# Kernel tuning notes

Hardware: AMD Instinct MI355X
Metric: run time of the kernel (lower is better)

The kernel has to match this reference:

```python
import jax, jax.numpy as jnp
import numpy as np

E = 512        # embedding_dim
HEADS = 8
PD = 32        # patch_dim
STRIDE = 16    # unfold stride (hard-coded in source)
P = 16         # max regions per image (padded)
NCLS = 3       # num_classes
LN_EPS = 1e-5


def layer_norm(x, g, b):
    mu = x.mean(-1, keepdims=True)
    v = ((x - mu) ** 2).mean(-1, keepdims=True)
    return (x - mu) / jnp.sqrt(v + LN_EPS) * g + b


def patch2vec(x, Wr, br):
    # x: [N, C, PD, PD]; AdaptiveAvgPool3d to (C//4, PD//2, PD//2) with exact
    # integer ratios == block-mean pooling, then Linear(fvector, E).
    N, C, H, W = x.shape
    y = x.reshape(N, C // 4, 4, H // 2, 2, W // 2, 2).mean(axis=(2, 4, 6))
    return y.reshape(N, -1) @ Wr.T + br


def mha(q_in, kv_in, Wqkv, bqkv, Wo, bo):
    # torch nn.MultiheadAttention, batch_first=True
    B, Pq, _ = q_in.shape
    L = kv_in.shape[1]
    hd = E // HEADS
    Wq, Wk, Wv = Wqkv[:E], Wqkv[E:2 * E], Wqkv[2 * E:]
    bq, bk, bv = bqkv[:E], bqkv[E:2 * E], bqkv[2 * E:]
    q = (q_in @ Wq.T + bq).reshape(B, Pq, HEADS, hd)
    k = (kv_in @ Wk.T + bk).reshape(B, L, HEADS, hd)
    v = (kv_in @ Wv.T + bv).reshape(B, L, HEADS, hd)
    scores = jnp.einsum('bphd,blhd->bhpl', q, k) / jnp.sqrt(jnp.asarray(hd, q.dtype))
    attn = jax.nn.softmax(scores, axis=-1)
    out = jnp.einsum('bhpl,blhd->bphd', attn, v).reshape(B, Pq, E)
    return out @ Wo.T + bo


def setup_inputs() -> dict:
    key = jax.random.key(0)
    ks = jax.random.split(key, 12)
    B, C, H, W = 8, 64, 256, 256
    fv = (C // 4) * (PD // 2) * (PD // 2)  # 4096
    s = lambda n: 1.0 / np.sqrt(n)
    return {
        'features': jax.random.normal(ks[0], (B, C, H, W), jnp.float32),
        'probs': jax.random.uniform(ks[1], (B, NCLS, H, W), jnp.float32),
        'patches': jax.random.normal(ks[2], (B, P, C, PD, PD), jnp.float32),
        'masks': jax.random.randint(ks[3], (B, H, W), 0, P + 1, jnp.int32),
        'ln_g': jnp.ones((E,), jnp.float32),
        'ln_b': jnp.zeros((E,), jnp.float32),
        'Wr': jax.random.normal(ks[4], (E, fv), jnp.float32) * s(fv),
        'br': jnp.zeros((E,), jnp.float32),
        'Wqkv': jax.random.normal(ks[5], (3 * E, E), jnp.float32) * s(E),
        'bqkv': jnp.zeros((3 * E,), jnp.float32),
        'Wo': jax.random.normal(ks[6], (E, E), jnp.float32) * s(E),
        'bo': jnp.zeros((E,), jnp.float32),
        'Wm': jax.random.normal(ks[7], (E, E), jnp.float32) * s(E),
        'bm': jnp.zeros((E,), jnp.float32),
        'Wc': jax.random.normal(ks[8], (NCLS - 1, E), jnp.float32) * s(E),
        'bc': jnp.zeros((NCLS - 1,), jnp.float32),
    }


def reference(features, probs, patches, masks, ln_g, ln_b, Wr, br,
              Wqkv, bqkv, Wo, bo, Wm, bm, Wc, bc):
    B, C, H, W = features.shape
    # ---- unfold features into overlapping PDxPD blocks, stride 16 ----
    n = (H - PD) // STRIDE + 1  # 15
    rows = (jnp.arange(n) * STRIDE)[:, None] + jnp.arange(PD)[None, :]  # [n, PD]
    xb = features[:, :, rows, :]          # [B, C, n, PD, W]
    blocks = xb[:, :, :, :, rows]         # [B, C, n, PD, n, PD]
    blocks = blocks.transpose(0, 2, 4, 1, 3, 5).reshape(B, n * n, C, PD, PD)
    L = n * n

    # ---- shared Patch2vec embedding + shared LayerNorm ----
    pe = layer_norm(patch2vec(patches.reshape(B * P, C, PD, PD), Wr, br).reshape(B, P, E), ln_g, ln_b)
    be = layer_norm(patch2vec(blocks.reshape(B * L, C, PD, PD), Wr, br).reshape(B, L, E), ln_g, ln_b)

    # ---- attention + residual MLP ----
    attn = mha(pe, be, Wqkv, bqkv, Wo, bo)
    res = layer_norm(attn + pe, ln_g, ln_b)
    x = jax.nn.gelu(res @ Wm.T + bm, approximate=False) + res
    outs = x @ Wc.T + bc  # [B, P, 2]

    # ---- vectorized masked reclassify (regions are disjoint) ----
    labels = masks  # [B, H, W], 0 = background, 1..P = regions
    seg = (labels.astype(jnp.int32) + jnp.arange(B, dtype=jnp.int32)[:, None, None] * (P + 1)).reshape(-1)
    pr = probs.transpose(0, 2, 3, 1).reshape(-1, NCLS)
    sums = jax.ops.segment_sum(pr, seg, num_segments=B * (P + 1)).reshape(B, P + 1, NCLS)
    cnt = jax.ops.segment_sum(jnp.ones((pr.shape[0],), pr.dtype), seg, num_segments=B * (P + 1)).reshape(B, P + 1)
    mean = sums / jnp.maximum(cnt, 1.0)[..., None] + 1e-6  # orig_mean_logits per region
    ml = mean[:, 1:, :]  # [B, P, NCLS], region labels 1..P <-> logits 0..P-1
    new0 = ml[..., 0] / (0.5 * (ml[..., 1] + ml[..., 2])) * outs.mean(-1)
    newv = jnp.stack([new0, outs[..., 0], outs[..., 1]], axis=-1)  # [B, P, 3]
    newv_full = jnp.concatenate([jnp.zeros((B, 1, NCLS), newv.dtype), newv], axis=1)
    vals = newv_full[jnp.arange(B)[:, None], labels.reshape(B, -1)]  # [B, H*W, 3]
    vals = vals.reshape(B, H, W, NCLS).transpose(0, 3, 1, 2)
    return jnp.where((labels > 0)[:, None, :, :], vals, probs)
```

## Files before the change

kernel.cpp:

```cpp
#include <hip/hip_runtime.h>
#include <stdint.h>


typedef __attribute__((ext_vector_type(8))) short bf16x8;
typedef __attribute__((ext_vector_type(4))) float f32x4;

__device__ __forceinline__ unsigned short f2bf(float x) {
    union { float f; unsigned u; } v; v.f = x;
    unsigned r = v.u + 0x7FFFu + ((v.u >> 16) & 1u);
    return (unsigned short)(r >> 16);
}
__device__ __forceinline__ float bf2f(unsigned short x) {
    union { unsigned u; float f; } v; v.u = ((unsigned)x) << 16; return v.f;
}

__device__ __forceinline__ void g2l16(const unsigned short* g, unsigned short* l) {
    __builtin_amdgcn_global_load_lds(
        (const __attribute__((address_space(1))) unsigned int*)g,
        (__attribute__((address_space(3))) unsigned int*)l, 16, 0, 0);
}

__global__ __launch_bounds__(256) void k_prep(
    const float* __restrict__ f, const float* __restrict__ p,
    const float* __restrict__ Wr, const float* __restrict__ Wqkv,
    const float* __restrict__ Wo, const float* __restrict__ Wm,
    unsigned short* __restrict__ gp, unsigned short* __restrict__ Xb,
    unsigned short* __restrict__ oWr, unsigned short* __restrict__ oWqkv,
    unsigned short* __restrict__ oWo, unsigned short* __restrict__ oWm,
    float* __restrict__ seg)
{
    int blk = blockIdx.x, tid = threadIdx.x;
    if (blk < 8192) {
        if (blk == 0) for (int i = tid; i < 544; i += 256) seg[i] = 0.f;
        unsigned t = blk * 256u + tid;
        unsigned q = t & 127u, r = (t >> 7) & 127u, g = (t >> 14) & 15u, b = t >> 18;
        const float2* f2 = (const float2*)f;
        float s = 0.f;
        unsigned cb = b * 64u + g * 4u;
#pragma unroll
        for (int j = 0; j < 4; ++j)
#pragma unroll
            for (int a = 0; a < 2; ++a) {
                unsigned idx = ((cb + j) * 256u + 2u * r + a) * 256u + 2u * q;
                float2 v = f2[idx >> 1];
                s += v.x + v.y;
            }
        gp[t] = f2bf(s * 0.0625f);
    } else if (blk < 10240) {
        unsigned t = (blk - 8192) * 256u + tid;
        unsigned i = t & 4095u, row = t >> 12;
        unsigned q = i & 15u, r = (i >> 4) & 15u, g = i >> 8;
        const float2* p2 = (const float2*)p;
        float s = 0.f;
        unsigned cb = row * 64u + g * 4u;
#pragma unroll
        for (int j = 0; j < 4; ++j)
#pragma unroll
            for (int a = 0; a < 2; ++a) {
                unsigned idx = ((cb + j) * 32u + 2u * r + a) * 32u + 2u * q;
                float2 v = p2[idx >> 1];
                s += v.x + v.y;
            }
        Xb[(size_t)row * 4096 + i] = f2bf(s * 0.0625f);
    } else {
        int t = (blk - 10240) * 256 + tid;
        const float* src; unsigned short* dst; int i;
        if (t < 524288)      { src = Wr;   dst = oWr;   i = t; }
        else if (t < 720896) { src = Wqkv; dst = oWqkv; i = t - 524288; }
        else if (t < 786432) { src = Wo;   dst = oWo;   i = t - 720896; }
        else                 { src = Wm;   dst = oWm;   i = t - 786432; }
        float4 v = ((const float4*)src)[i];
        ushort4 o;
        o.x = f2bf(v.x); o.y = f2bf(v.y); o.z = f2bf(v.z); o.w = f2bf(v.w);
        ((ushort4*)dst)[i] = o;
    }
}

__global__ __launch_bounds__(256) void k_gather_blocks(
    const unsigned short* __restrict__ Gp, unsigned short* __restrict__ Xb)
{
    unsigned t = blockIdx.x * 256u + threadIdx.x;
    unsigned grp = t & 511u, row_rel = t >> 9;
    unsigned k0 = grp * 8u;
    unsigned g = k0 >> 8, r = (k0 >> 4) & 15u, q0 = k0 & 15u;
    unsigned b = row_rel / 225u;
    unsigned ij = row_rel - b * 225u;
    unsigned i = ij / 15u, j = ij - i * 15u;
    size_t src = ((size_t)(b * 16u + g) * 128u + i * 8u + r) * 128u + j * 8u + q0;
    size_t dst = (size_t)(128u + row_rel) * 4096u + k0;
    *(uint4*)(Xb + dst) = *(const uint4*)(Gp + src);
}

__global__ __launch_bounds__(256) void k_gemm128(
    const unsigned short* __restrict__ A, const unsigned short* __restrict__ Bw,
    const float* __restrict__ bias, float* __restrict__ C,
    int M, int N, int K, int klen)
{
    __shared__ __align__(16) unsigned short As[128 * 32];
    __shared__ __align__(16) unsigned short Bs[128 * 32];
    const int tid = threadIdx.x, w = tid >> 6, lane = tid & 63;
    const int nt = blockIdx.x, mt = blockIdx.y, ks = blockIdx.z;
    const int kbase = ks * klen;
    const int l15 = lane & 15, kq = (lane >> 4) * 8;
    const int wm = (w >> 1) * 64, wn = (w & 1) * 64;
    const int srow0 = w * 32, lrow = lane >> 2, lcol = (lane & 3) * 8;

    f32x4 acc[4][4];
#pragma unroll
    for (int i = 0; i < 4; ++i)
#pragma unroll
        for (int j = 0; j < 4; ++j) acc[i][j] = (f32x4){0.f, 0.f, 0.f, 0.f};

    int arow0 = mt * 128, brow0 = nt * 128;
    for (int k0 = 0; k0 < klen; k0 += 32) {
        int kk = kbase + k0;
#pragma unroll
        for (int c = 0; c < 2; ++c) {
            int r = srow0 + c * 16 + lrow;
            int ga = arow0 + r; if (ga > M - 1) ga = M - 1;
            g2l16(A + (size_t)ga * K + kk + lcol, &As[(srow0 + c * 16) * 32]);
            g2l16(Bw + (size_t)(brow0 + r) * K + kk + lcol, &Bs[(srow0 + c * 16) * 32]);
        }
        __syncthreads();
        bf16x8 af[4], bf[4];
#pragma unroll
        for (int i = 0; i < 4; ++i) {
            af[i] = *(const bf16x8*)&As[(wm + 16 * i + l15) * 32 + kq];
            bf[i] = *(const bf16x8*)&Bs[(wn + 16 * i + l15) * 32 + kq];
        }
#pragma unroll
        for (int i = 0; i < 4; ++i)
#pragma unroll
            for (int j = 0; j < 4; ++j)
                acc[i][j] = __builtin_amdgcn_mfma_f32_16x16x32_bf16(af[i], bf[j], acc[i][j], 0, 0, 0);
        __syncthreads();
    }
    float* Cp = C + (size_t)ks * M * N;
#pragma unroll
    for (int i = 0; i < 4; ++i) {
        int rowb = mt * 128 + wm + i * 16 + (lane >> 4) * 4;
#pragma unroll
        for (int j = 0; j < 4; ++j) {
            int col = nt * 128 + wn + j * 16 + l15;
            float bv = bias ? bias[col] : 0.f;
#pragma unroll
            for (int r = 0; r < 4; ++r) {
                int row = rowb + r;
                if (row < M) Cp[(size_t)row * N + col] = acc[i][j][r] + bv;
            }
        }
    }
}

__global__ __launch_bounds__(256) void k_gemm_nt(
    const unsigned short* __restrict__ A, const unsigned short* __restrict__ Bw,
    const float* __restrict__ bias, float* __restrict__ C,
    int M, int N, int K)
{
    __shared__ __align__(16) unsigned short As[64 * 32];
    __shared__ __align__(16) unsigned short Bs[64 * 32];
    const int tid = threadIdx.x;
    const int bm = blockIdx.y, bn = blockIdx.x;
    const int wave = tid >> 6, lane = tid & 63;
    const int wm = (wave >> 1) * 32, wn = (wave & 1) * 32;
    const int l15 = lane & 15, kq = (lane >> 4) * 8;
    const int srow = tid >> 2, scol = (tid & 3) * 8;
    const unsigned short* Ap = A + (size_t)(bm * 64 + srow) * K + scol;
    const unsigned short* Bp = Bw + (size_t)(bn * 64 + srow) * K + scol;

    f32x4 acc[2][2];
#pragma unroll
    for (int i = 0; i < 2; ++i)
#pragma unroll
        for (int j = 0; j < 2; ++j) acc[i][j] = (f32x4){0.f, 0.f, 0.f, 0.f};

    for (int k0 = 0; k0 < K; k0 += 32) {
        *(uint4*)&As[srow * 32 + scol] = *(const uint4*)(Ap + k0);
        *(uint4*)&Bs[srow * 32 + scol] = *(const uint4*)(Bp + k0);
        __syncthreads();
        bf16x8 a0 = *(const bf16x8*)&As[(wm + l15) * 32 + kq];
        bf16x8 a1 = *(const bf16x8*)&As[(wm + 16 + l15) * 32 + kq];
        bf16x8 b0 = *(const bf16x8*)&Bs[(wn + l15) * 32 + kq];
        bf16x8 b1 = *(const bf16x8*)&Bs[(wn + 16 + l15) * 32 + kq];
        acc[0][0] = __builtin_amdgcn_mfma_f32_16x16x32_bf16(a0, b0, acc[0][0], 0, 0, 0);
        acc[0][1] = __builtin_amdgcn_mfma_f32_16x16x32_bf16(a0, b1, acc[0][1], 0, 0, 0);
        acc[1][0] = __builtin_amdgcn_mfma_f32_16x16x32_bf16(a1, b0, acc[1][0], 0, 0, 0);
        acc[1][1] = __builtin_amdgcn_mfma_f32_16x16x32_bf16(a1, b1, acc[1][1], 0, 0, 0);
        __syncthreads();
    }
#pragma unroll
    for (int it = 0; it < 2; ++it) {
        int rowb = bm * 64 + wm + it * 16 + (lane >> 4) * 4;
#pragma unroll
        for (int iu = 0; iu < 2; ++iu) {
            int col = bn * 64 + wn + iu * 16 + l15;
            float bv = bias[col];
#pragma unroll
            for (int r = 0; r < 4; ++r) {
                int row = rowb + r;
                if (row < M) C[(size_t)row * N + col] = acc[it][iu][r] + bv;
            }
        }
    }
}

__global__ __launch_bounds__(256) void k_lnred(
    const float* __restrict__ Yp, const float* __restrict__ br,
    const float* __restrict__ gg, const float* __restrict__ bb,
    float* __restrict__ outF, unsigned short* __restrict__ outB,
    int rows, int nsplit)
{
    int wave = threadIdx.x >> 6, lane = threadIdx.x & 63;
    int row = blockIdx.x * 4 + wave;
    if (row >= rows) return;
    size_t base = (size_t)row * 512 + lane * 8;
    float v[8];
    { const float* bp = br + lane * 8;
      float4 a = *(const float4*)bp, b = *(const float4*)(bp + 4);
      v[0]=a.x; v[1]=a.y; v[2]=a.z; v[3]=a.w; v[4]=b.x; v[5]=b.y; v[6]=b.z; v[7]=b.w; }
    for (int s = 0; s < nsplit; ++s) {
        const float* xp = Yp + (size_t)s * rows * 512 + base;
        float4 a = *(const float4*)xp, b = *(const float4*)(xp + 4);
        v[0]+=a.x; v[1]+=a.y; v[2]+=a.z; v[3]+=a.w; v[4]+=b.x; v[5]+=b.y; v[6]+=b.z; v[7]+=b.w;
    }
    float s = 0.f;
#pragma unroll
    for (int i = 0; i < 8; ++i) s += v[i];
#pragma unroll
    for (int m = 32; m; m >>= 1) s += __shfl_xor(s, m, 64);
    float mu = s * (1.f / 512.f);
    float sq = 0.f;
#pragma unroll
    for (int i = 0; i < 8; ++i) { float d = v[i] - mu; sq += d * d; }
#pragma unroll
    for (int m = 32; m; m >>= 1) sq += __shfl_xor(sq, m, 64);
    float rstd = rsqrtf(sq * (1.f / 512.f) + 1e-5f);
    const float* gp = gg + lane * 8;
    const float* bp2 = bb + lane * 8;
    float4 g0 = *(const float4*)gp, g1 = *(const float4*)(gp + 4);
    float4 b0 = *(const float4*)bp2, b1 = *(const float4*)(bp2 + 4);
    float ga[8] = {g0.x,g0.y,g0.z,g0.w,g1.x,g1.y,g1.z,g1.w};
    float ba[8] = {b0.x,b0.y,b0.z,b0.w,b1.x,b1.y,b1.z,b1.w};
    float o[8];
#pragma unroll
    for (int i = 0; i < 8; ++i) o[i] = (v[i] - mu) * rstd * ga[i] + ba[i];
    float* ofp = outF + base;
    float4 w0; w0.x=o[0]; w0.y=o[1]; w0.z=o[2]; w0.w=o[3];
    float4 w1; w1.x=o[4]; w1.y=o[5]; w1.z=o[6]; w1.w=o[7];
    *(float4*)ofp = w0; *(float4*)(ofp + 4) = w1;
    unsigned short* obp = outB + base;
    ushort4 u0, u1;
    u0.x=f2bf(o[0]); u0.y=f2bf(o[1]); u0.z=f2bf(o[2]); u0.w=f2bf(o[3]);
    u1.x=f2bf(o[4]); u1.y=f2bf(o[5]); u1.z=f2bf(o[6]); u1.w=f2bf(o[7]);
    ((ushort4*)obp)[0] = u0; ((ushort4*)obp)[1] = u1;
}

__global__ __launch_bounds__(256) void k_ln(
    const float* __restrict__ X, const float* __restrict__ R,
    const float* __restrict__ gg, const float* __restrict__ bb,
    float* __restrict__ outF, unsigned short* __restrict__ outB, int rows)
{
    int wave = threadIdx.x >> 6, lane = threadIdx.x & 63;
    int row = blockIdx.x * 4 + wave;
    if (row >= rows) return;
    size_t base = (size_t)row * 512 + lane * 8;
    const float* xp = X + base;
    float v[8];
    { float4 a = *(const float4*)xp, b = *(const float4*)(xp + 4);
      v[0]=a.x; v[1]=a.y; v[2]=a.z; v[3]=a.w; v[4]=b.x; v[5]=b.y; v[6]=b.z; v[7]=b.w; }
    { const float* rp = R + base;
      float4 a = *(const float4*)rp, b = *(const float4*)(rp + 4);
      v[0]+=a.x; v[1]+=a.y; v[2]+=a.z; v[3]+=a.w; v[4]+=b.x; v[5]+=b.y; v[6]+=b.z; v[7]+=b.w; }
    float s = 0.f;
#pragma unroll
    for (int i = 0; i < 8; ++i) s += v[i];
#pragma unroll
    for (int m = 32; m; m >>= 1) s += __shfl_xor(s, m, 64);
    float mu = s * (1.f / 512.f);
    float sq = 0.f;
#pragma unroll
    for (int i = 0; i < 8; ++i) { float d = v[i] - mu; sq += d * d; }
#pragma unroll
    for (int m = 32; m; m >>= 1) sq += __shfl_xor(sq, m, 64);
    float rstd = rsqrtf(sq * (1.f / 512.f) + 1e-5f);
    const float* gp = gg + lane * 8;
    const float* bp = bb + lane * 8;
    float4 g0 = *(const float4*)gp, g1 = *(const float4*)(gp + 4);
    float4 b0 = *(const float4*)bp, b1 = *(const float4*)(bp + 4);
    float ga[8] = {g0.x,g0.y,g0.z,g0.w,g1.x,g1.y,g1.z,g1.w};
    float ba[8] = {b0.x,b0.y,b0.z,b0.w,b1.x,b1.y,b1.z,b1.w};
    float o[8];
#pragma unroll
    for (int i = 0; i < 8; ++i) o[i] = (v[i] - mu) * rstd * ga[i] + ba[i];
    float* ofp = outF + base;
    float4 w0; w0.x=o[0]; w0.y=o[1]; w0.z=o[2]; w0.w=o[3];
    float4 w1; w1.x=o[4]; w1.y=o[5]; w1.z=o[6]; w1.w=o[7];
    *(float4*)ofp = w0; *(float4*)(ofp + 4) = w1;
    unsigned short* obp = outB + base;
    ushort4 u0, u1;
    u0.x=f2bf(o[0]); u0.y=f2bf(o[1]); u0.z=f2bf(o[2]); u0.w=f2bf(o[3]);
    u1.x=f2bf(o[4]); u1.y=f2bf(o[5]); u1.z=f2bf(o[6]); u1.w=f2bf(o[7]);
    ((ushort4*)obp)[0] = u0; ((ushort4*)obp)[1] = u1;
}

__global__ __launch_bounds__(256) void k_attn(
    const float* __restrict__ QKVp, const float* __restrict__ bqkv,
    unsigned short* __restrict__ attn_bf)
{
    const int b = blockIdx.x, h = blockIdx.y, pz = blockIdx.z;
    const size_t PS = (size_t)1928 * 1536;
    __shared__ __align__(16) float qs[4 * 64];
    __shared__ __align__(16) unsigned short Ks[225 * 68];
    __shared__ __align__(16) unsigned short Vs[225 * 64];
    __shared__ float sc[4 * 225];
    const int t = threadIdx.x;

    {
        int p = t >> 6, d = t & 63;
        size_t idx = (size_t)(b * 16 + pz * 4 + p) * 1536 + h * 64 + d;
        qs[t] = QKVp[idx] + QKVp[PS + idx] + bqkv[h * 64 + d];
    }
    float bk = bqkv[512 + h * 64 + (t & 63)];
    float bv = bqkv[1024 + h * 64 + (t & 63)];
    for (int i = t; i < 14400; i += 256) {
        int l = i >> 6, d = i & 63;
        size_t base = (size_t)(128 + b * 225 + l) * 1536 + h * 64 + d;
        Ks[l * 68 + d] = f2bf(QKVp[base + 512] + QKVp[PS + base + 512] + bk);
        Vs[l * 64 + d] = f2bf(QKVp[base + 1024] + QKVp[PS + base + 1024] + bv);
    }
    __syncthreads();
    for (int i = t; i < 900; i += 256) {
        int p = i / 225, l = i - p * 225;
        const ushort4* k4 = (const ushort4*)&Ks[l * 68];
        const float4* q4 = (const float4*)&qs[p * 64];
        float s = 0.f;
#pragma unroll
        for (int d = 0; d < 16; ++d) {
            ushort4 kk = k4[d]; float4 qq = q4[d];
            s += bf2f(kk.x) * qq.x + bf2f(kk.y) * qq.y
               + bf2f(kk.z) * qq.z + bf2f(kk.w) * qq.w;
        }
        sc[p * 225 + l] = s * 0.125f;
    }
    __syncthreads();
    const int lane = t & 63, wave = t >> 6;
    {
        float* row = &sc[wave * 225];
        float m = -1e30f;
        for (int l = lane; l < 225; l += 64) m = fmaxf(m, row[l]);
#pragma unroll
        for (int off = 32; off; off >>= 1) m = fmaxf(m, __shfl_xor(m, off, 64));
        float s = 0.f;
        for (int l = lane; l < 225; l += 64) { float e = __expf(row[l] - m); row[l] = e; s += e; }
#pragma unroll
        for (int off = 32; off; off >>= 1) s += __shfl_xor(s, off, 64);
        float inv = 1.f / s;
        for (int l = lane; l < 225; l += 64) row[l] *= inv;
    }
    __syncthreads();
    {
        float o = 0.f;
        const float* scp = &sc[wave * 225];
        for (int l = 0; l < 225; ++l) o += scp[l] * bf2f(Vs[l * 64 + lane]);
        attn_bf[(size_t)(b * 16 + pz * 4 + wave) * 512 + h * 64 + lane] = f2bf(o);
    }
}

__global__ __launch_bounds__(256) void k_wc(
    const float* __restrict__ m1, const float* __restrict__ res,
    const float* __restrict__ Wc, const float* __restrict__ bc,
    float* __restrict__ outs)
{
    int wave = threadIdx.x >> 6, lane = threadIdx.x & 63;
    int row = blockIdx.x * 4 + wave;
    size_t base = (size_t)row * 512 + lane * 8;
    const float* mp = m1 + base;
    const float* rp = res + base;
    const float* w0p = Wc + lane * 8;
    const float* w1p = Wc + 512 + lane * 8;
    float4 ma = *(const float4*)mp, mb = *(const float4*)(mp + 4);
    float4 ra = *(const float4*)rp, rb = *(const float4*)(rp + 4);
    float4 wa0 = *(const float4*)w0p, wb0 = *(const float4*)(w0p + 4);
    float4 wa1 = *(const float4*)w1p, wb1 = *(const float4*)(w1p + 4);
    float mv[8] = {ma.x,ma.y,ma.z,ma.w,mb.x,mb.y,mb.z,mb.w};
    float rv[8] = {ra.x,ra.y,ra.z,ra.w,rb.x,rb.y,rb.z,rb.w};
    float w0[8] = {wa0.x,wa0.y,wa0.z,wa0.w,wb0.x,wb0.y,wb0.z,wb0.w};
    float w1[8] = {wa1.x,wa1.y,wa1.z,wa1.w,wb1.x,wb1.y,wb1.z,wb1.w};
    float s0 = 0.f, s1 = 0.f;
#pragma unroll
    for (int i = 0; i < 8; ++i) {
        float v = mv[i];
        float x = 0.5f * v * (1.f + erff(v * 0.70710678118654752f)) + rv[i];
        s0 += x * w0[i]; s1 += x * w1[i];
    }
#pragma unroll
    for (int m = 32; m; m >>= 1) {
        s0 += __shfl_xor(s0, m, 64);
        s1 += __shfl_xor(s1, m, 64);
    }
    if (lane == 0) {
        outs[row * 2 + 0] = s0 + bc[0];
        outs[row * 2 + 1] = s1 + bc[1];
    }
}

__global__ __launch_bounds__(256) void k_hist(
    const int* __restrict__ masks, const float* __restrict__ probs,
    float* __restrict__ sums, float* __restrict__ cnt)
{
    __shared__ float ls[4][68];
    int t = threadIdx.x, wave = t >> 6;
    for (int i = t; i < 272; i += 256) ((float*)ls)[i] = 0.f;
    __syncthreads();
    int b = blockIdx.x >> 6, chunk = blockIdx.x & 63;
    int base = chunk * 1024;
    for (int it = 0; it < 4; ++it) {
        int px = base + it * 256 + t;
        int lab = masks[b * 65536 + px];
        atomicAdd(&ls[wave][lab * 3 + 0], probs[(size_t)(b * 3 + 0) * 65536 + px]);
        atomicAdd(&ls[wave][lab * 3 + 1], probs[(size_t)(b * 3 + 1) * 65536 + px]);
        atomicAdd(&ls[wave][lab * 3 + 2], probs[(size_t)(b * 3 + 2) * 65536 + px]);
        atomicAdd(&ls[wave][51 + lab], 1.f);
    }
    __syncthreads();
    if (t < 68) {
        float v = ls[0][t] + ls[1][t] + ls[2][t] + ls[3][t];
        if (t < 51) atomicAdd(&sums[b * 51 + t], v);
        else        atomicAdd(&cnt[b * 17 + t - 51], v);
    }
}

__global__ __launch_bounds__(256) void k_out(
    const int* __restrict__ masks, const float* __restrict__ probs,
    const float* __restrict__ seg, const float* __restrict__ outs,
    float* __restrict__ out)
{
    __shared__ float nv[17 * 3];
    int tid = threadIdx.x;
    int b = blockIdx.x >> 8;
    if (tid < 17) {
        int lab = tid;
        if (lab == 0) { nv[0] = 0.f; nv[1] = 0.f; nv[2] = 0.f; }
        else {
            float c  = fmaxf(seg[408 + b * 17 + lab], 1.f);
            float m0 = seg[(b * 17 + lab) * 3 + 0] / c + 1e-6f;
            float m1 = seg[(b * 17 + lab) * 3 + 1] / c + 1e-6f;
            float m2 = seg[(b * 17 + lab) * 3 + 2] / c + 1e-6f;
            int p = lab - 1;
            float o0 = outs[(b * 16 + p) * 2 + 0], o1 = outs[(b * 16 + p) * 2 + 1];
            nv[lab * 3 + 0] = m0 / (0.5f * (m1 + m2)) * (0.5f * (o0 + o1));
            nv[lab * 3 + 1] = o0;
            nv[lab * 3 + 2] = o1;
        }
    }
    __syncthreads();
    int px = (blockIdx.x & 255) * 256 + tid;
    int gl = b * 65536 + px;
    int lab = masks[gl];
    if (lab > 0) {
        out[(size_t)(b*3+0)*65536 + px] = nv[lab*3+0];
        out[(size_t)(b*3+1)*65536 + px] = nv[lab*3+1];
        out[(size_t)(b*3+2)*65536 + px] = nv[lab*3+2];
    } else {
        out[(size_t)(b*3+0)*65536 + px] = probs[(size_t)(b*3+0)*65536 + px];
        out[(size_t)(b*3+1)*65536 + px] = probs[(size_t)(b*3+1)*65536 + px];
        out[(size_t)(b*3+2)*65536 + px] = probs[(size_t)(b*3+2)*65536 + px];
    }
}

extern "C" void kernel_launch(void* const* d_in, const int* in_sizes, int n_in,
                              void* d_out, int out_size, void* d_ws, size_t ws_size,
                              hipStream_t stream)
{
    const float* features = (const float*)d_in[0];
    const float* probs    = (const float*)d_in[1];
    const float* patches  = (const float*)d_in[2];
    const int*   masks    = (const int*)d_in[3];
    const float* ln_g     = (const float*)d_in[4];
    const float* ln_b     = (const float*)d_in[5];
    const float* Wr       = (const float*)d_in[6];
    const float* br       = (const float*)d_in[7];
    const float* Wqkv     = (const float*)d_in[8];
    const float* bqkv     = (const float*)d_in[9];
    const float* Wo       = (const float*)d_in[10];
    const float* bo       = (const float*)d_in[11];
    const float* Wm       = (const float*)d_in[12];
    const float* bm       = (const float*)d_in[13];
    const float* Wc       = (const float*)d_in[14];
    const float* bc       = (const float*)d_in[15];
    float* out = (float*)d_out;

    char* w = (char*)d_ws;
    size_t off = 0;
    auto alloc = [&](size_t bytes) -> char* {
        char* p = w + off;
        off += (bytes + 255) & ~(size_t)255;
        return p;
    };
    unsigned short* Gp     = (unsigned short*)alloc((size_t)2097152 * 2);
    unsigned short* Xb     = (unsigned short*)alloc((size_t)1928 * 4096 * 2);
    unsigned short* Wr_b   = (unsigned short*)alloc((size_t)2097152 * 2);
    unsigned short* Wqkv_b = (unsigned short*)alloc((size_t)786432 * 2);
    unsigned short* Wo_b   = (unsigned short*)alloc((size_t)262144 * 2);
    unsigned short* Wm_b   = (unsigned short*)alloc((size_t)262144 * 2);
    float* Yp   = (float*)alloc((size_t)8 * 1928 * 512 * 4);
    float* LNf  = (float*)alloc((size_t)1928 * 512 * 4);
    unsigned short* LNb = (unsigned short*)alloc((size_t)1928 * 512 * 2);
    float* QKV  = (float*)alloc((size_t)2 * 1928 * 1536 * 4);
    unsigned short* attnb = (unsigned short*)alloc((size_t)65536 * 2);
    float* Zo   = (float*)alloc((size_t)65536 * 4);
    float* resf = (float*)alloc((size_t)65536 * 4);
    unsigned short* resb = (unsigned short*)alloc((size_t)65536 * 2);
    float* M1   = (float*)alloc((size_t)65536 * 4);
    float* outsB = (float*)alloc((size_t)256 * 4);
    float* seg   = (float*)alloc((size_t)544 * 4);

    k_prep<<<13568, 256, 0, stream>>>(features, patches, Wr, Wqkv, Wo, Wm,
                                      Gp, Xb, Wr_b, Wqkv_b, Wo_b, Wm_b, seg);
    k_gather_blocks<<<3600, 256, 0, stream>>>(Gp, Xb);
    k_gemm128<<<dim3(4, 16, 8), 256, 0, stream>>>(Xb, Wr_b, nullptr, Yp, 1928, 512, 4096, 512);
    k_lnred<<<482, 256, 0, stream>>>(Yp, br, ln_g, ln_b, LNf, LNb, 1928, 8);
    k_gemm128<<<dim3(12, 16, 2), 256, 0, stream>>>(LNb, Wqkv_b, nullptr, QKV, 1928, 1536, 512, 256);
    k_attn<<<dim3(8, 8, 4), 256, 0, stream>>>(QKV, bqkv, attnb);
    k_gemm_nt<<<dim3(8, 2), 256, 0, stream>>>(attnb, Wo_b, bo, Zo, 128, 512, 512);
    k_ln<<<32, 256, 0, stream>>>(Zo, LNf, ln_g, ln_b, resf, resb, 128);
    k_gemm_nt<<<dim3(8, 2), 256, 0, stream>>>(resb, Wm_b, bm, M1, 128, 512, 512);
    k_wc<<<32, 256, 0, stream>>>(M1, resf, Wc, bc, outsB);
    k_hist<<<512, 256, 0, stream>>>(masks, probs, seg, seg + 408);
    k_out<<<2048, 256, 0, stream>>>(masks, probs, seg, outsB, out);
}
```

Measured before the change: 368.0 us.

## Fuse patch gather into GEMM, drop QKV split-K, fuse attention tail into one kernel

The separate gather kernel that copied unfolded patch rows into Xb is removed, and the Wr GEMM now computes those source addresses in Gp directly, which saves a full 1800x4096 bf16 write and read. The QKV GEMM no longer uses split-K, so bias is applied in the epilogue and the attention kernel reads one buffer instead of summing two partials. The output projection, residual LayerNorm, MLP GEMM, GELU and classifier run in a single 8-block kernel instead of five launches. The histogram kernel moves earlier in the stream. The cost is low parallelism in the fused tail, with only 8 blocks, and a QKV GEMM with fewer blocks and a longer K loop.

```diff
diff --git a/kernel.cpp b/kernel.cpp
--- a/kernel.cpp
+++ b/kernel.cpp
@@ -76,23 +76,10 @@
     }
 }
 
-__global__ __launch_bounds__(256) void k_gather_blocks(
-    const unsigned short* __restrict__ Gp, unsigned short* __restrict__ Xb)
-{
-    unsigned t = blockIdx.x * 256u + threadIdx.x;
-    unsigned grp = t & 511u, row_rel = t >> 9;
-    unsigned k0 = grp * 8u;
-    unsigned g = k0 >> 8, r = (k0 >> 4) & 15u, q0 = k0 & 15u;
-    unsigned b = row_rel / 225u;
-    unsigned ij = row_rel - b * 225u;
-    unsigned i = ij / 15u, j = ij - i * 15u;
-    size_t src = ((size_t)(b * 16u + g) * 128u + i * 8u + r) * 128u + j * 8u + q0;
-    size_t dst = (size_t)(128u + row_rel) * 4096u + k0;
-    *(uint4*)(Xb + dst) = *(const uint4*)(Gp + src);
-}
-
+template<bool GATHER>
 __global__ __launch_bounds__(256) void k_gemm128(
-    const unsigned short* __restrict__ A, const unsigned short* __restrict__ Bw,
+    const unsigned short* __restrict__ A, const unsigned short* __restrict__ Gp,
+    const unsigned short* __restrict__ Bw,
     const float* __restrict__ bias, float* __restrict__ C,
     int M, int N, int K, int klen)
 {
@@ -105,21 +92,45 @@
     const int wm = (w >> 1) * 64, wn = (w & 1) * 64;
     const int srow0 = w * 32, lrow = lane >> 2, lcol = (lane & 3) * 8;
 
+    size_t arowbase[2]; bool apatch[2];
+#pragma unroll
+    for (int c = 0; c < 2; ++c) {
+        int r = srow0 + c * 16 + lrow;
+        int ga = mt * 128 + r; if (ga > M - 1) ga = M - 1;
+        if (GATHER && ga >= 128) {
+            int rr = ga - 128;
+            int bb = rr / 225, ij = rr - bb * 225;
+            int ii = ij / 15, jj = ij - ii * 15;
+            arowbase[c] = (size_t)bb * 262144 + ii * 1024 + jj * 8;
+            apatch[c] = false;
+        } else {
+            arowbase[c] = (size_t)ga * K;
+            apatch[c] = true;
+        }
+    }
+    const int brow0 = nt * 128;
+
     f32x4 acc[4][4];
 #pragma unroll
     for (int i = 0; i < 4; ++i)
 #pragma unroll
         for (int j = 0; j < 4; ++j) acc[i][j] = (f32x4){0.f, 0.f, 0.f, 0.f};
 
-    int arow0 = mt * 128, brow0 = nt * 128;
     for (int k0 = 0; k0 < klen; k0 += 32) {
         int kk = kbase + k0;
+        int kcol = kk + lcol;
 #pragma unroll
         for (int c = 0; c < 2; ++c) {
-            int r = srow0 + c * 16 + lrow;
-            int ga = arow0 + r; if (ga > M - 1) ga = M - 1;
-            g2l16(A + (size_t)ga * K + kk + lcol, &As[(srow0 + c * 16) * 32]);
-            g2l16(Bw + (size_t)(brow0 + r) * K + kk + lcol, &Bs[(srow0 + c * 16) * 32]);
+            const unsigned short* gp_a;
+            if (!GATHER || apatch[c]) {
+                gp_a = A + arowbase[c] + kcol;
+            } else {
+                gp_a = Gp + arowbase[c] + ((size_t)(kcol >> 8) << 14)
+                     + (((kcol >> 4) & 15) << 7) + (kcol & 15);
+            }
+            g2l16(gp_a, &As[(srow0 + c * 16) * 32]);
+            g2l16(Bw + (size_t)(brow0 + srow0 + c * 16 + lrow) * K + kcol,
+                  &Bs[(srow0 + c * 16) * 32]);
         }
         __syncthreads();
         bf16x8 af[4], bf[4];
@@ -147,58 +158,6 @@
             for (int r = 0; r < 4; ++r) {
                 int row = rowb + r;
                 if (row < M) Cp[(size_t)row * N + col] = acc[i][j][r] + bv;
-            }
-        }
-    }
-}
-
-__global__ __launch_bounds__(256) void k_gemm_nt(
-    const unsigned short* __restrict__ A, const unsigned short* __restrict__ Bw,
-    const float* __restrict__ bias, float* __restrict__ C,
-    int M, int N, int K)
-{
-    __shared__ __align__(16) unsigned short As[64 * 32];
-    __shared__ __align__(16) unsigned short Bs[64 * 32];
-    const int tid = threadIdx.x;
-    const int bm = blockIdx.y, bn = blockIdx.x;
-    const int wave = tid >> 6, lane = tid & 63;
-    const int wm = (wave >> 1) * 32, wn = (wave & 1) * 32;
-    const int l15 = lane & 15, kq = (lane >> 4) * 8;
-    const int srow = tid >> 2, scol = (tid & 3) * 8;
-    const unsigned short* Ap = A + (size_t)(bm * 64 + srow) * K + scol;
-    const unsigned short* Bp = Bw + (size_t)(bn * 64 + srow) * K + scol;
-
-    f32x4 acc[2][2];
-#pragma unroll
-    for (int i = 0; i < 2; ++i)
-#pragma unroll
-        for (int j = 0; j < 2; ++j) acc[i][j] = (f32x4){0.f, 0.f, 0.f, 0.f};
-
-    for (int k0 = 0; k0 < K; k0 += 32) {
-        *(uint4*)&As[srow * 32 + scol] = *(const uint4*)(Ap + k0);
-        *(uint4*)&Bs[srow * 32 + scol] = *(const uint4*)(Bp + k0);
-        __syncthreads();
-        bf16x8 a0 = *(const bf16x8*)&As[(wm + l15) * 32 + kq];
-        bf16x8 a1 = *(const bf16x8*)&As[(wm + 16 + l15) * 32 + kq];
-        bf16x8 b0 = *(const bf16x8*)&Bs[(wn + l15) * 32 + kq];
-        bf16x8 b1 = *(const bf16x8*)&Bs[(wn + 16 + l15) * 32 + kq];
-        acc[0][0] = __builtin_amdgcn_mfma_f32_16x16x32_bf16(a0, b0, acc[0][0], 0, 0, 0);
-        acc[0][1] = __builtin_amdgcn_mfma_f32_16x16x32_bf16(a0, b1, acc[0][1], 0, 0, 0);
-        acc[1][0] = __builtin_amdgcn_mfma_f32_16x16x32_bf16(a1, b0, acc[1][0], 0, 0, 0);
-        acc[1][1] = __builtin_amdgcn_mfma_f32_16x16x32_bf16(a1, b1, acc[1][1], 0, 0, 0);
-        __syncthreads();
-    }
-#pragma unroll
-    for (int it = 0; it < 2; ++it) {
-        int rowb = bm * 64 + wm + it * 16 + (lane >> 4) * 4;
-#pragma unroll
-        for (int iu = 0; iu < 2; ++iu) {
-            int col = bn * 64 + wn + iu * 16 + l15;
-            float bv = bias[col];
-#pragma unroll
-            for (int r = 0; r < 4; ++r) {
-                int row = rowb + r;
-                if (row < M) C[(size_t)row * N + col] = acc[it][iu][r] + bv;
             }
         }
     }
@@ -255,60 +214,10 @@
     ((ushort4*)obp)[0] = u0; ((ushort4*)obp)[1] = u1;
 }
 
-__global__ __launch_bounds__(256) void k_ln(
-    const float* __restrict__ X, const float* __restrict__ R,
-    const float* __restrict__ gg, const float* __restrict__ bb,
-    float* __restrict__ outF, unsigned short* __restrict__ outB, int rows)
-{
-    int wave = threadIdx.x >> 6, lane = threadIdx.x & 63;
-    int row = blockIdx.x * 4 + wave;
-    if (row >= rows) return;
-    size_t base = (size_t)row * 512 + lane * 8;
-    const float* xp = X + base;
-    float v[8];
-    { float4 a = *(const float4*)xp, b = *(const float4*)(xp + 4);
-      v[0]=a.x; v[1]=a.y; v[2]=a.z; v[3]=a.w; v[4]=b.x; v[5]=b.y; v[6]=b.z; v[7]=b.w; }
-    { const float* rp = R + base;
-      float4 a = *(const float4*)rp, b = *(const float4*)(rp + 4);
-      v[0]+=a.x; v[1]+=a.y; v[2]+=a.z; v[3]+=a.w; v[4]+=b.x; v[5]+=b.y; v[6]+=b.z; v[7]+=b.w; }
-    float s = 0.f;
-#pragma unroll
-    for (int i = 0; i < 8; ++i) s += v[i];
-#pragma unroll
-    for (int m = 32; m; m >>= 1) s += __shfl_xor(s, m, 64);
-    float mu = s * (1.f / 512.f);
-    float sq = 0.f;
-#pragma unroll
-    for (int i = 0; i < 8; ++i) { float d = v[i] - mu; sq += d * d; }
-#pragma unroll
-    for (int m = 32; m; m >>= 1) sq += __shfl_xor(sq, m, 64);
-    float rstd = rsqrtf(sq * (1.f / 512.f) + 1e-5f);
-    const float* gp = gg + lane * 8;
-    const float* bp = bb + lane * 8;
-    float4 g0 = *(const float4*)gp, g1 = *(const float4*)(gp + 4);
-    float4 b0 = *(const float4*)bp, b1 = *(const float4*)(bp + 4);
-    float ga[8] = {g0.x,g0.y,g0.z,g0.w,g1.x,g1.y,g1.z,g1.w};
-    float ba[8] = {b0.x,b0.y,b0.z,b0.w,b1.x,b1.y,b1.z,b1.w};
-    float o[8];
-#pragma unroll
-    for (int i = 0; i < 8; ++i) o[i] = (v[i] - mu) * rstd * ga[i] + ba[i];
-    float* ofp = outF + base;
-    float4 w0; w0.x=o[0]; w0.y=o[1]; w0.z=o[2]; w0.w=o[3];
-    float4 w1; w1.x=o[4]; w1.y=o[5]; w1.z=o[6]; w1.w=o[7];
-    *(float4*)ofp = w0; *(float4*)(ofp + 4) = w1;
-    unsigned short* obp = outB + base;
-    ushort4 u0, u1;
-    u0.x=f2bf(o[0]); u0.y=f2bf(o[1]); u0.z=f2bf(o[2]); u0.w=f2bf(o[3]);
-    u1.x=f2bf(o[4]); u1.y=f2bf(o[5]); u1.z=f2bf(o[6]); u1.w=f2bf(o[7]);
-    ((ushort4*)obp)[0] = u0; ((ushort4*)obp)[1] = u1;
-}
-
 __global__ __launch_bounds__(256) void k_attn(
-    const float* __restrict__ QKVp, const float* __restrict__ bqkv,
-    unsigned short* __restrict__ attn_bf)
+    const float* __restrict__ QKV, unsigned short* __restrict__ attn_bf)
 {
     const int b = blockIdx.x, h = blockIdx.y, pz = blockIdx.z;
-    const size_t PS = (size_t)1928 * 1536;
     __shared__ __align__(16) float qs[4 * 64];
     __shared__ __align__(16) unsigned short Ks[225 * 68];
     __shared__ __align__(16) unsigned short Vs[225 * 64];
@@ -317,16 +226,13 @@
 
     {
         int p = t >> 6, d = t & 63;
-        size_t idx = (size_t)(b * 16 + pz * 4 + p) * 1536 + h * 64 + d;
-        qs[t] = QKVp[idx] + QKVp[PS + idx] + bqkv[h * 64 + d];
-    }
-    float bk = bqkv[512 + h * 64 + (t & 63)];
-    float bv = bqkv[1024 + h * 64 + (t & 63)];
+        qs[t] = QKV[(size_t)(b * 16 + pz * 4 + p) * 1536 + h * 64 + d];
+    }
     for (int i = t; i < 14400; i += 256) {
         int l = i >> 6, d = i & 63;
         size_t base = (size_t)(128 + b * 225 + l) * 1536 + h * 64 + d;
-        Ks[l * 68 + d] = f2bf(QKVp[base + 512] + QKVp[PS + base + 512] + bk);
-        Vs[l * 64 + d] = f2bf(QKVp[base + 1024] + QKVp[PS + base + 1024] + bv);
+        Ks[l * 68 + d] = f2bf(QKV[base + 512]);
+        Vs[l * 64 + d] = f2bf(QKV[base + 1024]);
     }
     __syncthreads();
     for (int i = t; i < 900; i += 256) {
@@ -366,41 +272,133 @@
     }
 }
 
-__global__ __launch_bounds__(256) void k_wc(
-    const float* __restrict__ m1, const float* __restrict__ res,
+__global__ __launch_bounds__(256) void k_tail(
+    const unsigned short* __restrict__ attnb, const unsigned short* __restrict__ Wo_b,
+    const float* __restrict__ bo, const float* __restrict__ LNf,
+    const float* __restrict__ gg, const float* __restrict__ bb,
+    const unsigned short* __restrict__ Wm_b, const float* __restrict__ bm,
     const float* __restrict__ Wc, const float* __restrict__ bc,
     float* __restrict__ outs)
 {
-    int wave = threadIdx.x >> 6, lane = threadIdx.x & 63;
-    int row = blockIdx.x * 4 + wave;
-    size_t base = (size_t)row * 512 + lane * 8;
-    const float* mp = m1 + base;
-    const float* rp = res + base;
-    const float* w0p = Wc + lane * 8;
-    const float* w1p = Wc + 512 + lane * 8;
-    float4 ma = *(const float4*)mp, mb = *(const float4*)(mp + 4);
-    float4 ra = *(const float4*)rp, rb = *(const float4*)(rp + 4);
-    float4 wa0 = *(const float4*)w0p, wb0 = *(const float4*)(w0p + 4);
-    float4 wa1 = *(const float4*)w1p, wb1 = *(const float4*)(w1p + 4);
-    float mv[8] = {ma.x,ma.y,ma.z,ma.w,mb.x,mb.y,mb.z,mb.w};
-    float rv[8] = {ra.x,ra.y,ra.z,ra.w,rb.x,rb.y,rb.z,rb.w};
-    float w0[8] = {wa0.x,wa0.y,wa0.z,wa0.w,wb0.x,wb0.y,wb0.z,wb0.w};
-    float w1[8] = {wa1.x,wa1.y,wa1.z,wa1.w,wb1.x,wb1.y,wb1.z,wb1.w};
-    float s0 = 0.f, s1 = 0.f;
+    __shared__ __align__(16) unsigned short Abuf[16 * 520];
+    __shared__ __align__(16) unsigned short Bs[4][128 * 32];
+    __shared__ float Zf[16 * 512];
+    __shared__ float part[16][4][2];
+    const int tid = threadIdx.x, w = tid >> 6, lane = tid & 63;
+    const int l15 = lane & 15, quad = lane >> 4, kq = quad * 8;
+    const int r0 = blockIdx.x * 16;
+
+#pragma unroll
+    for (int c = 0; c < 4; ++c) {
+        int row = c * 4 + w;
+        g2l16(attnb + (size_t)(r0 + row) * 512 + lane * 8, &Abuf[row * 520]);
+    }
+
+    f32x4 acc[8];
+#pragma unroll
+    for (int i = 0; i < 8; ++i) acc[i] = (f32x4){0.f, 0.f, 0.f, 0.f};
+
+    for (int k0 = 0; k0 < 512; k0 += 32) {
+#pragma unroll
+        for (int c = 0; c < 8; ++c) {
+            int n = w * 128 + c * 16 + (lane >> 2);
+            g2l16(Wo_b + (size_t)n * 512 + k0 + (lane & 3) * 8, &Bs[w][(c * 16) * 32]);
+        }
+        __syncthreads();
+        bf16x8 af = *(const bf16x8*)&Abuf[l15 * 520 + k0 + kq];
+#pragma unroll
+        for (int i = 0; i < 8; ++i) {
+            bf16x8 bf = *(const bf16x8*)&Bs[w][(i * 16 + l15) * 32 + kq];
+            acc[i] = __builtin_amdgcn_mfma_f32_16x16x32_bf16(af, bf, acc[i], 0, 0, 0);
+        }
+        __syncthreads();
+    }
 #pragma unroll
     for (int i = 0; i < 8; ++i) {
-        float v = mv[i];
-        float x = 0.5f * v * (1.f + erff(v * 0.70710678118654752f)) + rv[i];
-        s0 += x * w0[i]; s1 += x * w1[i];
-    }
-#pragma unroll
-    for (int m = 32; m; m >>= 1) {
-        s0 += __shfl_xor(s0, m, 64);
-        s1 += __shfl_xor(s1, m, 64);
-    }
-    if (lane == 0) {
-        outs[row * 2 + 0] = s0 + bc[0];
-        outs[row * 2 + 1] = s1 + bc[1];
+        int col = w * 128 + i * 16 + l15;
+        float bv = bo[col];
+#pragma unroll
+        for (int r = 0; r < 4; ++r)
+            Zf[(quad * 4 + r) * 512 + col] = acc[i][r] + bv;
+    }
+    __syncthreads();
+
+    for (int pass = 0; pass < 4; ++pass) {
+        int row = pass * 4 + w;
+        float v[8];
+#pragma unroll
+        for (int i = 0; i < 8; ++i)
+            v[i] = Zf[row * 512 + lane * 8 + i] + LNf[(size_t)(r0 + row) * 512 + lane * 8 + i];
+        float s = 0.f;
+#pragma unroll
+        for (int i = 0; i < 8; ++i) s += v[i];
+#pragma unroll
+        for (int m = 32; m; m >>= 1) s += __shfl_xor(s, m, 64);
+        float mu = s * (1.f / 512.f);
+        float sq = 0.f;
+#pragma unroll
+        for (int i = 0; i < 8; ++i) { float d = v[i] - mu; sq += d * d; }
+#pragma unroll
+        for (int m = 32; m; m >>= 1) sq += __shfl_xor(sq, m, 64);
+        float rstd = rsqrtf(sq * (1.f / 512.f) + 1e-5f);
+#pragma unroll
+        for (int i = 0; i < 8; ++i) {
+            int col = lane * 8 + i;
+            float o = (v[i] - mu) * rstd * gg[col] + bb[col];
+            Zf[row * 512 + col] = o;
+            Abuf[row * 520 + col] = f2bf(o);
+        }
+    }
+    __syncthreads();
+
+#pragma unroll
+    for (int i = 0; i < 8; ++i) acc[i] = (f32x4){0.f, 0.f, 0.f, 0.f};
+    for (int k0 = 0; k0 < 512; k0 += 32) {
+#pragma unroll
+        for (int c = 0; c < 8; ++c) {
+            int n = w * 128 + c * 16 + (lane >> 2);
+            g2l16(Wm_b + (size_t)n * 512 + k0 + (lane & 3) * 8, &Bs[w][(c * 16) * 32]);
+        }
+        __syncthreads();
+        bf16x8 af = *(const bf16x8*)&Abuf[l15 * 520 + k0 + kq];
+#pragma unroll
+        for (int i = 0; i < 8; ++i) {
+            bf16x8 bf = *(const bf16x8*)&Bs[w][(i * 16 + l15) * 32 + kq];
+            acc[i] = __builtin_amdgcn_mfma_f32_16x16x32_bf16(af, bf, acc[i], 0, 0, 0);
+        }
+        __syncthreads();
+    }
+    float s0[4] = {0,0,0,0}, s1[4] = {0,0,0,0};
+#pragma unroll
+    for (int i = 0; i < 8; ++i) {
+        int col = w * 128 + i * 16 + l15;
+        float wc0 = Wc[col], wc1 = Wc[512 + col], bmv = bm[col];
+#pragma unroll
+        for (int r = 0; r < 4; ++r) {
+            float v = acc[i][r] + bmv;
+            float x = 0.5f * v * (1.f + erff(v * 0.70710678118654752f))
+                    + Zf[(quad * 4 + r) * 512 + col];
+            s0[r] += x * wc0; s1[r] += x * wc1;
+        }
+    }
+#pragma unroll
+    for (int off = 8; off; off >>= 1)
+#pragma unroll
+        for (int r = 0; r < 4; ++r) {
+            s0[r] += __shfl_xor(s0[r], off, 16);
+            s1[r] += __shfl_xor(s1[r], off, 16);
+        }
+    if (l15 == 0)
+#pragma unroll
+        for (int r = 0; r < 4; ++r) {
+            part[quad * 4 + r][w][0] = s0[r];
+            part[quad * 4 + r][w][1] = s1[r];
+        }
+    __syncthreads();
+    if (tid < 32) {
+        int row = tid >> 1, c = tid & 1;
+        float s = part[row][0][c] + part[row][1][c] + part[row][2][c] + part[row][3][c];
+        outs[(r0 + row) * 2 + c] = s + bc[c];
     }
 }
 
@@ -498,7 +496,7 @@
         return p;
     };
     unsigned short* Gp     = (unsigned short*)alloc((size_t)2097152 * 2);
-    unsigned short* Xb     = (unsigned short*)alloc((size_t)1928 * 4096 * 2);
+    unsigned short* Xb     = (unsigned short*)alloc((size_t)128 * 4096 * 2);
     unsigned short* Wr_b   = (unsigned short*)alloc((size_t)2097152 * 2);
     unsigned short* Wqkv_b = (unsigned short*)alloc((size_t)786432 * 2);
     unsigned short* Wo_b   = (unsigned short*)alloc((size_t)262144 * 2);
@@ -506,26 +504,21 @@
     float* Yp   = (float*)alloc((size_t)8 * 1928 * 512 * 4);
     float* LNf  = (float*)alloc((size_t)1928 * 512 * 4);
     unsigned short* LNb = (unsigned short*)alloc((size_t)1928 * 512 * 2);
-    float* QKV  = (float*)alloc((size_t)2 * 1928 * 1536 * 4);
+    float* QKV  = (float*)alloc((size_t)1928 * 1536 * 4);
     unsigned short* attnb = (unsigned short*)alloc((size_t)65536 * 2);
-    float* Zo   = (float*)alloc((size_t)65536 * 4);
-    float* resf = (float*)alloc((size_t)65536 * 4);
-    unsigned short* resb = (unsigned short*)alloc((size_t)65536 * 2);
-    float* M1   = (float*)alloc((size_t)65536 * 4);
     float* outsB = (float*)alloc((size_t)256 * 4);
     float* seg   = (float*)alloc((size_t)544 * 4);
 
     k_prep<<<13568, 256, 0, stream>>>(features, patches, Wr, Wqkv, Wo, Wm,
                                       Gp, Xb, Wr_b, Wqkv_b, Wo_b, Wm_b, seg);
-    k_gather_blocks<<<3600, 256, 0, stream>>>(Gp, Xb);
-    k_gemm128<<<dim3(4, 16, 8), 256, 0, stream>>>(Xb, Wr_b, nullptr, Yp, 1928, 512, 4096, 512);
+    k_hist<<<512, 256, 0, stream>>>(masks, probs, seg, seg + 408);
+    k_gemm128<true><<<dim3(4, 16, 8), 256, 0, stream>>>(
+        Xb, Gp, Wr_b, nullptr, Yp, 1928, 512, 4096, 512);
     k_lnred<<<482, 256, 0, stream>>>(Yp, br, ln_g, ln_b, LNf, LNb, 1928, 8);
-    k_gemm128<<<dim3(12, 16, 2), 256, 0, stream>>>(LNb, Wqkv_b, nullptr, QKV, 1928, 1536, 512, 256);
-    k_attn<<<dim3(8, 8, 4), 256, 0, stream>>>(QKV, bqkv, attnb);
-    k_gemm_nt<<<dim3(8, 2), 256, 0, stream>>>(attnb, Wo_b, bo, Zo, 128, 512, 512);
-    k_ln<<<32, 256, 0, stream>>>(Zo, LNf, ln_g, ln_b, resf, resb, 128);
-    k_gemm_nt<<<dim3(8, 2), 256, 0, stream>>>(resb, Wm_b, bm, M1, 128, 512, 512);
-    k_wc<<<32, 256, 0, stream>>>(M1, resf, Wc, bc, outsB);
-    k_hist<<<512, 256, 0, stream>>>(masks, probs, seg, seg + 408);
+    k_gemm128<false><<<dim3(12, 16, 1), 256, 0, stream>>>(
+        LNb, nullptr, Wqkv_b, bqkv, QKV, 1928, 1536, 512, 512);
+    k_attn<<<dim3(8, 8, 4), 256, 0, stream>>>(QKV, attnb);
+    k_tail<<<8, 256, 0, stream>>>(attnb, Wo_b, bo, LNf, ln_g, ln_b,
+                                  Wm_b, bm, Wc, bc, outsB);
     k_out<<<2048, 256, 0, stream>>>(masks, probs, seg, outsB, out);
 }
```

Result: no change. 370.6 us (+0.7%).
